# Kernel tuning notes

Measured on AMD Instinct MI355X. Metric: run time of the kernel, lower is better.

The kernel has to match this reference:

```python
import jax, jax.numpy as jnp
import numpy as np

B, S, D, H = 2, 2048, 1024, 16
HD = D // H
SCALE = HD ** -0.5

def setup_inputs() -> dict:
    key = jax.random.key(0)
    ks = jax.random.split(key, 5)
    x = jax.random.normal(ks[0], (B, S, D), dtype=jnp.float32)
    Wqkv = jax.random.normal(ks[1], (D, 3 * D), dtype=jnp.float32) * (D ** -0.5)
    bqkv = jnp.zeros((3 * D,), dtype=jnp.float32)
    Wproj = jax.random.normal(ks[2], (D, D), dtype=jnp.float32) * (D ** -0.5)
    bproj = jnp.zeros((D,), dtype=jnp.float32)
    return {"x": x, "Wqkv": Wqkv, "bqkv": bqkv, "Wproj": Wproj, "bproj": bproj}

def reference(x, Wqkv, bqkv, Wproj, bproj):
    b, s, _ = x.shape
    qkv = x @ Wqkv + bqkv                       # [B,S,3D]
    qkv = qkv.reshape(b, s, 3, H, HD)
    q, k, v = [jnp.transpose(qkv[:, :, i], (0, 2, 1, 3)) for i in range(3)]  # [B,H,S,HD]
    attn = jnp.einsum('bhqd,bhkd->bhqk', q, k) * SCALE   # [B,H,S,S]
    attn = jax.nn.softmax(attn, axis=-1)
    out = jnp.einsum('bhqk,bhkd->bhqd', attn, v)         # [B,H,S,HD]
    out = jnp.transpose(out, (0, 2, 1, 3)).reshape(b, s, D)
    return out @ Wproj + bproj
```

## Files before the change

kernel.cpp:

```cpp
#include <hip/hip_runtime.h>
#include <hip/hip_bf16.h>

#define BB 2
#define SS 2048
#define DD 1024
#define HH 16
#define HDD 64
#define MM (BB*SS)
#define NQKV (3*DD)
#define SCALE 0.125f
#define QPRESCALE 0.18033688f

typedef __bf16 bf16_t;
typedef bf16_t bf16x4 __attribute__((ext_vector_type(4)));
typedef bf16_t bf16x8 __attribute__((ext_vector_type(8)));
typedef float f32x4 __attribute__((ext_vector_type(4)));
typedef float f32x16 __attribute__((ext_vector_type(16)));

__device__ __forceinline__ void gl_lds16(const bf16_t* g, bf16_t* l) {
    __builtin_amdgcn_global_load_lds(
        (const __attribute__((address_space(1))) unsigned int*)(uintptr_t)g,
        (__attribute__((address_space(3))) unsigned int*)(uintptr_t)l,
        16, 0, 0);
}

__global__ __launch_bounds__(256) void prep(
    const float* __restrict__ x, const float* __restrict__ Wqkv,
    const float* __restrict__ Wproj, bf16_t* __restrict__ xb,
    bf16_t* __restrict__ wqkvt, bf16_t* __restrict__ wprojt)
{
    const int bx = blockIdx.x;
    if (bx < 2048) {
        int i = (bx * 256 + threadIdx.x) * 8;
        float4 a = *(const float4*)(x + i);
        float4 b = *(const float4*)(x + i + 4);
        bf16x8 v;
        v[0]=(bf16_t)a.x; v[1]=(bf16_t)a.y; v[2]=(bf16_t)a.z; v[3]=(bf16_t)a.w;
        v[4]=(bf16_t)b.x; v[5]=(bf16_t)b.y; v[6]=(bf16_t)b.z; v[7]=(bf16_t)b.w;
        *reinterpret_cast<bf16x8*>(xb + i) = v;
        return;
    }
    __shared__ float tile[32][33];
    const float* src; bf16_t* dst; int C, bxl, byl;
    if (bx < 5120) {
        int t = bx - 2048;
        byl = t / 96; bxl = t - byl * 96;
        src = Wqkv;  dst = wqkvt;  C = NQKV;
    } else {
        int t = bx - 5120;
        byl = t >> 5; bxl = t & 31;
        src = Wproj; dst = wprojt; C = DD;
    }
    const int R = DD;
    const int tx = threadIdx.x & 31, ty = threadIdx.x >> 5;
    const int r0 = byl * 32, c0 = bxl * 32;
    #pragma unroll
    for (int i = 0; i < 32; i += 8)
        tile[ty + i][tx] = src[(size_t)(r0 + ty + i) * C + c0 + tx];
    __syncthreads();
    #pragma unroll
    for (int i = 0; i < 32; i += 8)
        dst[(size_t)(c0 + ty + i) * R + r0 + tx] = (bf16_t)tile[tx][ty + i];
}

template <int MODE>
__global__ __launch_bounds__(256) void gemm_bt(
    const bf16_t* __restrict__ A, const bf16_t* __restrict__ Bt,
    const float* __restrict__ bias, float* __restrict__ outf,
    bf16_t* __restrict__ qw, bf16_t* __restrict__ kw, bf16_t* __restrict__ vtw,
    int N, int K)
{
    __shared__ __align__(16) bf16_t As[128 * 32];
    __shared__ __align__(16) bf16_t Bs[128 * 32];

    const int tid  = threadIdx.x;
    const int w    = tid >> 6;
    const int lane = tid & 63;
    const int lr   = lane & 15;
    const int quad = lane >> 4;
    const int m0   = blockIdx.y * 128;
    const int n0   = blockIdx.x * 128;
    const int wm   = w >> 1;
    const int wn   = w & 1;

    f32x4 acc[4][4];
    #pragma unroll
    for (int i = 0; i < 4; i++)
        #pragma unroll
        for (int j = 0; j < 4; j++) acc[i][j] = (f32x4){0.f, 0.f, 0.f, 0.f};

    const int stgRow = lane >> 2;
    const int stgCol = (lane & 3) * 8;
    const bf16_t* aPtr = A  + (size_t)(m0 + w * 32 + stgRow) * K + stgCol;
    const bf16_t* bPtr = Bt + (size_t)(n0 + w * 32 + stgRow) * K + stgCol;
    bf16_t* aDst = As + w * 1024;
    bf16_t* bDst = Bs + w * 1024;
    const size_t rowSkip = (size_t)16 * K;

    for (int ks = 0; ks < K; ks += 32) {
        __syncthreads();
        gl_lds16(aPtr + ks,           aDst);
        gl_lds16(aPtr + rowSkip + ks, aDst + 512);
        gl_lds16(bPtr + ks,           bDst);
        gl_lds16(bPtr + rowSkip + ks, bDst + 512);
        __syncthreads();

        bf16x8 af[4], bf[4];
        #pragma unroll
        for (int mi = 0; mi < 4; mi++)
            af[mi] = *reinterpret_cast<const bf16x8*>(&As[(wm * 64 + mi * 16 + lr) * 32 + quad * 8]);
        #pragma unroll
        for (int ni = 0; ni < 4; ni++)
            bf[ni] = *reinterpret_cast<const bf16x8*>(&Bs[(wn * 64 + ni * 16 + lr) * 32 + quad * 8]);
        #pragma unroll
        for (int mi = 0; mi < 4; mi++)
            #pragma unroll
            for (int ni = 0; ni < 4; ni++)
                acc[mi][ni] = __builtin_amdgcn_mfma_f32_16x16x32_bf16(af[mi], bf[ni], acc[mi][ni], 0, 0, 0);
    }

    #pragma unroll
    for (int mi = 0; mi < 4; mi++) {
        #pragma unroll
        for (int ni = 0; ni < 4; ni++) {
            #pragma unroll
            for (int reg = 0; reg < 4; reg++) {
                int row = m0 + wm * 64 + mi * 16 + quad * 4 + reg;
                int col = n0 + wn * 64 + ni * 16 + lr;
                float val = acc[mi][ni][reg] + bias[col];
                if constexpr (MODE == 0) {
                    int b = row >> 11, s = row & 2047;
                    int which = col >> 10, d = col & 1023;
                    int h = d >> 6, hd = d & 63;
                    size_t bh = (size_t)(b * HH + h);
                    if (which == 0)      qw[(bh * SS + s) * HDD + hd] = (bf16_t)(val * QPRESCALE);
                    else if (which == 1) kw[(bh * SS + s) * HDD + hd] = (bf16_t)val;
                    else                 vtw[(bh * HDD + hd) * SS + s] = (bf16_t)val;
                } else {
                    outf[(size_t)row * N + col] = val;
                }
            }
        }
    }
}

__global__ __launch_bounds__(256) void gemm_bt64(
    const bf16_t* __restrict__ A, const bf16_t* __restrict__ Bt,
    const float* __restrict__ bias, float* __restrict__ outf, int N, int K)
{
    __shared__ __align__(16) bf16_t As[2][64 * 32];
    __shared__ __align__(16) bf16_t Bs[2][128 * 32];

    const int tid  = threadIdx.x;
    const int w    = tid >> 6;
    const int lane = tid & 63;
    const int lr   = lane & 15;
    const int quad = lane >> 4;
    const int m0   = blockIdx.y * 64;
    const int n0   = blockIdx.x * 128;
    const int wm   = w >> 1;
    const int wn   = w & 1;

    f32x4 acc[2][4];
    #pragma unroll
    for (int i = 0; i < 2; i++)
        #pragma unroll
        for (int j = 0; j < 4; j++) acc[i][j] = (f32x4){0.f, 0.f, 0.f, 0.f};

    const int stgRow = lane >> 2;
    const int stgCol = (lane & 3) * 8;
    const bf16_t* aPtr = A  + (size_t)(m0 + w * 16 + stgRow) * K + stgCol;
    const bf16_t* bPtr = Bt + (size_t)(n0 + w * 32 + stgRow) * K + stgCol;
    const size_t rowSkip = (size_t)16 * K;

    for (int ks = 0; ks < K; ks += 64) {
        __syncthreads();
        #pragma unroll
        for (int s = 0; s < 2; s++) {
            const int ko = ks + s * 32;
            gl_lds16(aPtr + ko,           &As[s][w * 512]);
            gl_lds16(bPtr + ko,           &Bs[s][w * 1024]);
            gl_lds16(bPtr + rowSkip + ko, &Bs[s][w * 1024 + 512]);
        }
        __syncthreads();

        #pragma unroll
        for (int s = 0; s < 2; s++) {
            bf16x8 af[2], bf[4];
            #pragma unroll
            for (int mi = 0; mi < 2; mi++)
                af[mi] = *reinterpret_cast<const bf16x8*>(&As[s][(wm * 32 + mi * 16 + lr) * 32 + quad * 8]);
            #pragma unroll
            for (int ni = 0; ni < 4; ni++)
                bf[ni] = *reinterpret_cast<const bf16x8*>(&Bs[s][(wn * 64 + ni * 16 + lr) * 32 + quad * 8]);
            #pragma unroll
            for (int mi = 0; mi < 2; mi++)
                #pragma unroll
                for (int ni = 0; ni < 4; ni++)
                    acc[mi][ni] = __builtin_amdgcn_mfma_f32_16x16x32_bf16(af[mi], bf[ni], acc[mi][ni], 0, 0, 0);
        }
    }

    #pragma unroll
    for (int mi = 0; mi < 2; mi++)
        #pragma unroll
        for (int ni = 0; ni < 4; ni++)
            #pragma unroll
            for (int reg = 0; reg < 4; reg++) {
                int row = m0 + wm * 32 + mi * 16 + quad * 4 + reg;
                int col = n0 + wn * 64 + ni * 16 + lr;
                outf[(size_t)row * N + col] = acc[mi][ni][reg] + bias[col];
            }
}

__global__ __launch_bounds__(512, 4) void attn_kernel(
    const bf16_t* __restrict__ qws, const bf16_t* __restrict__ kws,
    const bf16_t* __restrict__ vtws, bf16_t* __restrict__ ob)
{
    __shared__ __align__(16) bf16_t smem[34048];
    bf16_t* Ks = smem;
    bf16_t* Vs = smem + 16640;

    const int tid  = threadIdx.x;
    const int w    = tid >> 6;
    const int g    = w >> 2;
    const int wg   = w & 3;
    const int lane = tid & 63;
    const int ln31 = lane & 31;
    const int ln5  = lane >> 5;

    const int qb = blockIdx.x;
    const int bh = blockIdx.y;
    const int b  = bh >> 4;
    const int h  = bh & 15;

    const bf16_t* Qh  = qws  + (size_t)bh * SS * HDD;
    const bf16_t* Kh  = kws  + (size_t)bh * SS * HDD;
    const bf16_t* Vth = vtws + (size_t)bh * HDD * SS;

    const int q0w    = qb * 128 + wg * 32;
    const int kvbase = g * 1024;

    bf16x8 aq[4];
    #pragma unroll
    for (int f = 0; f < 4; f++)
        aq[f] = *(const bf16x8*)(Qh + (size_t)(q0w + ln31) * HDD + f * 16 + ln5 * 8);

    const int gtid = tid & 255;
    const int sc = gtid & 7;
    const int sr = gtid >> 3;

    {
        const int ko = g * 520;
        const int vo = g * 4352;
        bf16x8 k0 = *(const bf16x8*)(Kh  + (size_t)(kvbase + sr     ) * HDD + sc * 8);
        bf16x8 k1 = *(const bf16x8*)(Kh  + (size_t)(kvbase + sr + 32) * HDD + sc * 8);
        bf16x8 v0 = *(const bf16x8*)(Vth + (size_t)(sr     ) * SS + kvbase + sc * 8);
        bf16x8 v1 = *(const bf16x8*)(Vth + (size_t)(sr + 32) * SS + kvbase + sc * 8);
        *reinterpret_cast<bf16x8*>(&Ks[(ko + sc * 65 + sr     ) * 8]) = k0;
        *reinterpret_cast<bf16x8*>(&Ks[(ko + sc * 65 + sr + 32) * 8]) = k1;
        bf16_t* vd0 = &Vs[vo + (sr     ) * 68 + sc * 8];
        bf16_t* vd1 = &Vs[vo + (sr + 32) * 68 + sc * 8];
        *reinterpret_cast<bf16x4*>(vd0)     = __builtin_shufflevector(v0, v0, 0,1,2,3);
        *reinterpret_cast<bf16x4*>(vd0 + 4) = __builtin_shufflevector(v0, v0, 4,5,6,7);
        *reinterpret_cast<bf16x4*>(vd1)     = __builtin_shufflevector(v1, v1, 0,1,2,3);
        *reinterpret_cast<bf16x4*>(vd1 + 4) = __builtin_shufflevector(v1, v1, 4,5,6,7);
    }
    __syncthreads();

    float l = 0.f;
    f32x16 o[2];
    #pragma unroll
    for (int nh = 0; nh < 2; nh++)
        #pragma unroll
        for (int r = 0; r < 16; r++) o[nh][r] = 0.f;

    int buf = 0;
    for (int it = 0; it < 16; ++it) {
        const int ko = buf * 1040 + g * 520;
        const int vo = buf * 8704 + g * 4352;

        f32x16 sfr[2];
        #pragma unroll
        for (int ni = 0; ni < 2; ni++) {
            #pragma unroll
            for (int r = 0; r < 16; r++) sfr[ni][r] = 0.f;
            #pragma unroll
            for (int f = 0; f < 4; f++) {
                bf16x8 kb = *reinterpret_cast<const bf16x8*>(
                    &Ks[(ko + (2 * f + ln5) * 65 + ni * 32 + ln31) * 8]);
                sfr[ni] = __builtin_amdgcn_mfma_f32_32x32x16_bf16(kb, aq[f], sfr[ni], 0, 0, 0);
            }
        }

        bf16x8 nk0, nk1, nv0, nv1;
        const bool more = (it + 1 < 16);
        if (more) {
            const int kvn = kvbase + (it + 1) * 64;
            nk0 = *(const bf16x8*)(Kh  + (size_t)(kvn + sr     ) * HDD + sc * 8);
            nk1 = *(const bf16x8*)(Kh  + (size_t)(kvn + sr + 32) * HDD + sc * 8);
            nv0 = *(const bf16x8*)(Vth + (size_t)(sr     ) * SS + kvn + sc * 8);
            nv1 = *(const bf16x8*)(Vth + (size_t)(sr + 32) * SS + kvn + sc * 8);
        }

        float p[2][16];
        #pragma unroll
        for (int ni = 0; ni < 2; ni++)
            #pragma unroll
            for (int r = 0; r < 16; r++) {
                p[ni][r] = __builtin_amdgcn_exp2f(sfr[ni][r]);
                l += p[ni][r];
            }

        bf16x8 ap[4];
        #pragma unroll
        for (int c16 = 0; c16 < 4; c16++)
            #pragma unroll
            for (int j = 0; j < 8; j++)
                ap[c16][j] = (bf16_t)p[c16 >> 1][(c16 & 1) * 8 + j];

        #pragma unroll
        for (int nh = 0; nh < 2; nh++) {
            const bf16_t* vrow = &Vs[vo + (nh * 32 + ln31) * 68];
            #pragma unroll
            for (int c16 = 0; c16 < 4; c16++) {
                bf16x4 lo = *(const bf16x4*)(vrow + c16 * 16 + 4 * ln5);
                bf16x4 hi = *(const bf16x4*)(vrow + c16 * 16 + 8 + 4 * ln5);
                bf16x8 vb = __builtin_shufflevector(lo, hi, 0, 1, 2, 3, 4, 5, 6, 7);
                o[nh] = __builtin_amdgcn_mfma_f32_32x32x16_bf16(ap[c16], vb, o[nh], 0, 0, 0);
            }
        }

        if (more) {
            const int ko1 = (buf ^ 1) * 1040 + g * 520;
            const int vo1 = (buf ^ 1) * 8704 + g * 4352;
            *reinterpret_cast<bf16x8*>(&Ks[(ko1 + sc * 65 + sr     ) * 8]) = nk0;
            *reinterpret_cast<bf16x8*>(&Ks[(ko1 + sc * 65 + sr + 32) * 8]) = nk1;
            bf16_t* vd0 = &Vs[vo1 + (sr     ) * 68 + sc * 8];
            bf16_t* vd1 = &Vs[vo1 + (sr + 32) * 68 + sc * 8];
            *reinterpret_cast<bf16x4*>(vd0)     = __builtin_shufflevector(nv0, nv0, 0,1,2,3);
            *reinterpret_cast<bf16x4*>(vd0 + 4) = __builtin_shufflevector(nv0, nv0, 4,5,6,7);
            *reinterpret_cast<bf16x4*>(vd1)     = __builtin_shufflevector(nv1, nv1, 0,1,2,3);
            *reinterpret_cast<bf16x4*>(vd1 + 4) = __builtin_shufflevector(nv1, nv1, 4,5,6,7);
        }
        __syncthreads();
        buf ^= 1;
    }

    l += __shfl_xor(l, 32, 64);

    __syncthreads();
    float* Of = (float*)smem;
    float* Lf = (float*)(smem + 16384);
    if (ln5 == 0) Lf[g * 128 + wg * 32 + ln31] = l;
    if (g == 1) {
        #pragma unroll
        for (int nh = 0; nh < 2; nh++)
            #pragma unroll
            for (int r = 0; r < 16; r++) {
                const int q = (r & 3) + 8 * (r >> 2) + 4 * ln5;
                Of[(wg * 32 + q) * 64 + nh * 32 + ln31] = o[nh][r];
            }
    }
    __syncthreads();
    if (g == 0) {
        float inv[16];
        #pragma unroll
        for (int r = 0; r < 16; r++) {
            const int q = (r & 3) + 8 * (r >> 2) + 4 * ln5;
            inv[r] = 1.f / (Lf[wg * 32 + q] + Lf[128 + wg * 32 + q]);
        }
        #pragma unroll
        for (int nh = 0; nh < 2; nh++)
            #pragma unroll
            for (int r = 0; r < 16; r++) {
                const int q  = (r & 3) + 8 * (r >> 2) + 4 * ln5;
                const int hd = nh * 32 + ln31;
                float val = (o[nh][r] + Of[(wg * 32 + q) * 64 + hd]) * inv[r];
                ob[((size_t)b * SS + q0w + q) * DD + h * HDD + hd] = (bf16_t)val;
            }
    }
}

extern "C" void kernel_launch(void* const* d_in, const int* in_sizes, int n_in,
                              void* d_out, int out_size, void* d_ws, size_t ws_size,
                              hipStream_t stream) {
    const float* x     = (const float*)d_in[0];
    const float* Wqkv  = (const float*)d_in[1];
    const float* bqkv  = (const float*)d_in[2];
    const float* Wproj = (const float*)d_in[3];
    const float* bproj = (const float*)d_in[4];
    float* out = (float*)d_out;

    const size_t NEL = (size_t)MM * DD;
    bf16_t* qws    = (bf16_t*)d_ws;
    bf16_t* kws    = qws  + NEL;
    bf16_t* vtws   = kws  + NEL;
    bf16_t* xb     = vtws + NEL;
    bf16_t* ows    = xb;
    bf16_t* wqkvt  = xb + NEL;
    bf16_t* wprojt = wqkvt + (size_t)NQKV * DD;

    prep<<<6144, 256, 0, stream>>>(x, Wqkv, Wproj, xb, wqkvt, wprojt);

    gemm_bt<0><<<dim3(NQKV / 128, MM / 128), 256, 0, stream>>>(
        xb, wqkvt, bqkv, nullptr, qws, kws, vtws, NQKV, DD);

    attn_kernel<<<dim3(SS / 128, BB * HH), 512, 0, stream>>>(qws, kws, vtws, ows);

    gemm_bt64<<<dim3(DD / 128, MM / 64), 256, 0, stream>>>(
        ows, wprojt, bproj, out, DD, DD);
}
```

Measured before the change: 187.6 us.

## Rewrite QKV GEMM with 256x192 tiles, double-buffered swizzled LDS and interleaved prefetch

Replaces the simple 128x128, BK=32 QKV GEMM, which synchronised twice per step with no overlap, with a 512-thread kernel using 256x192 block tiles and BK=64. LDS is double-buffered, and the next tile's global-to-LDS loads are issued in between MFMA phases. An XOR swizzle is added to avoid LDS bank conflicts, and s_setprio is raised around the MFMA bursts. The grid shrinks to 16x16=256 blocks, which roughly matches the CU count but adds wave quantisation risk, along with larger LDS use (~112KB) and higher register pressure.

Measured after the change: 192.5 us. +2.6%, slower.

```diff
diff --git a/kernel.cpp b/kernel.cpp
--- a/kernel.cpp
+++ b/kernel.cpp
@@ -22,6 +22,10 @@
         (const __attribute__((address_space(1))) unsigned int*)(uintptr_t)g,
         (__attribute__((address_space(3))) unsigned int*)(uintptr_t)l,
         16, 0, 0);
+}
+
+__device__ __forceinline__ f32x4 MF(bf16x8 a, bf16x8 b, f32x4 c) {
+    return __builtin_amdgcn_mfma_f32_16x16x32_bf16(a, b, c, 0, 0, 0);
 }
 
 __global__ __launch_bounds__(256) void prep(
@@ -63,81 +67,171 @@
         dst[(size_t)(c0 + ty + i) * R + r0 + tx] = (bf16_t)tile[tx][ty + i];
 }
 
-template <int MODE>
-__global__ __launch_bounds__(256) void gemm_bt(
+__global__ __launch_bounds__(512, 2) void gemm_qkv(
     const bf16_t* __restrict__ A, const bf16_t* __restrict__ Bt,
-    const float* __restrict__ bias, float* __restrict__ outf,
-    bf16_t* __restrict__ qw, bf16_t* __restrict__ kw, bf16_t* __restrict__ vtw,
-    int N, int K)
+    const float* __restrict__ bias,
+    bf16_t* __restrict__ qw, bf16_t* __restrict__ kw, bf16_t* __restrict__ vtw)
 {
-    __shared__ __align__(16) bf16_t As[128 * 32];
-    __shared__ __align__(16) bf16_t Bs[128 * 32];
+    constexpr int K  = DD;
+    constexpr int BM = 256, BN = 192, BK = 64;
+    constexpr int NT = K / BK;
+
+    __shared__ __align__(16) bf16_t smem[2 * BM * BK + 2 * BN * BK];
+    bf16_t* const As0 = smem;
+    bf16_t* const As1 = smem + BM * BK;
+    bf16_t* const Bs0 = smem + 2 * BM * BK;
+    bf16_t* const Bs1 = Bs0 + BN * BK;
 
     const int tid  = threadIdx.x;
     const int w    = tid >> 6;
     const int lane = tid & 63;
     const int lr   = lane & 15;
     const int quad = lane >> 4;
-    const int m0   = blockIdx.y * 128;
-    const int n0   = blockIdx.x * 128;
-    const int wm   = w >> 1;
-    const int wn   = w & 1;
-
-    f32x4 acc[4][4];
-    #pragma unroll
-    for (int i = 0; i < 4; i++)
-        #pragma unroll
-        for (int j = 0; j < 4; j++) acc[i][j] = (f32x4){0.f, 0.f, 0.f, 0.f};
-
-    const int stgRow = lane >> 2;
-    const int stgCol = (lane & 3) * 8;
-    const bf16_t* aPtr = A  + (size_t)(m0 + w * 32 + stgRow) * K + stgCol;
-    const bf16_t* bPtr = Bt + (size_t)(n0 + w * 32 + stgRow) * K + stgCol;
-    bf16_t* aDst = As + w * 1024;
-    bf16_t* bDst = Bs + w * 1024;
-    const size_t rowSkip = (size_t)16 * K;
-
-    for (int ks = 0; ks < K; ks += 32) {
-        __syncthreads();
-        gl_lds16(aPtr + ks,           aDst);
-        gl_lds16(aPtr + rowSkip + ks, aDst + 512);
-        gl_lds16(bPtr + ks,           bDst);
-        gl_lds16(bPtr + rowSkip + ks, bDst + 512);
-        __syncthreads();
-
-        bf16x8 af[4], bf[4];
-        #pragma unroll
-        for (int mi = 0; mi < 4; mi++)
-            af[mi] = *reinterpret_cast<const bf16x8*>(&As[(wm * 64 + mi * 16 + lr) * 32 + quad * 8]);
-        #pragma unroll
-        for (int ni = 0; ni < 4; ni++)
-            bf[ni] = *reinterpret_cast<const bf16x8*>(&Bs[(wn * 64 + ni * 16 + lr) * 32 + quad * 8]);
-        #pragma unroll
-        for (int mi = 0; mi < 4; mi++)
-            #pragma unroll
-            for (int ni = 0; ni < 4; ni++)
-                acc[mi][ni] = __builtin_amdgcn_mfma_f32_16x16x32_bf16(af[mi], bf[ni], acc[mi][ni], 0, 0, 0);
-    }
-
-    #pragma unroll
-    for (int mi = 0; mi < 4; mi++) {
-        #pragma unroll
-        for (int ni = 0; ni < 4; ni++) {
-            #pragma unroll
-            for (int reg = 0; reg < 4; reg++) {
-                int row = m0 + wm * 64 + mi * 16 + quad * 4 + reg;
-                int col = n0 + wn * 64 + ni * 16 + lr;
-                float val = acc[mi][ni][reg] + bias[col];
-                if constexpr (MODE == 0) {
-                    int b = row >> 11, s = row & 2047;
-                    int which = col >> 10, d = col & 1023;
-                    int h = d >> 6, hd = d & 63;
-                    size_t bh = (size_t)(b * HH + h);
+    const int wm   = w >> 2;
+    const int wn   = w & 3;
+    const int m0   = blockIdx.y * BM;
+    const int n0   = blockIdx.x * BN;
+
+    const int sx   = lr & 7;
+    const int ecc0 = ((quad)     ^ sx) * 8;
+    const int ecc1 = ((quad + 4) ^ sx) * 8;
+    const int aOff = (wm * 128 + lr) * BK;
+    const int bOff = (wn * 48  + lr) * BK;
+
+    f32x4 acc[2][4][3];
+    #pragma unroll
+    for (int mh = 0; mh < 2; mh++)
+        #pragma unroll
+        for (int mi = 0; mi < 4; mi++)
+            #pragma unroll
+            for (int ni = 0; ni < 3; ni++)
+                acc[mh][mi][ni] = (f32x4){0.f, 0.f, 0.f, 0.f};
+
+    auto stageA = [&](int kt, bf16_t* dst) {
+        #pragma unroll
+        for (int r = 0; r < 4; ++r) {
+            const int c   = r * 512 + tid;
+            const int row = c >> 3;
+            const int cg  = (c & 7) ^ (row & 7);
+            gl_lds16(A + (size_t)(m0 + row) * K + kt * BK + cg * 8, dst + c * 8);
+        }
+    };
+    auto stageB = [&](int kt, bf16_t* dst) {
+        #pragma unroll
+        for (int r = 0; r < 3; ++r) {
+            const int c   = r * 512 + tid;
+            const int row = c >> 3;
+            const int cg  = (c & 7) ^ (row & 7);
+            gl_lds16(Bt + (size_t)(n0 + row) * K + kt * BK + cg * 8, dst + c * 8);
+        }
+    };
+
+    stageA(0, As0);
+    stageB(0, Bs0);
+    asm volatile("s_waitcnt vmcnt(0)" ::: "memory");
+    __builtin_amdgcn_s_barrier();
+
+    auto tile = [&](int t, const bf16_t* Ac, const bf16_t* Bc,
+                    bf16_t* An, bf16_t* Bn) {
+        const bool more = (t + 1) < NT;
+        bf16x8 af[4], bk0[3], bk1[3];
+
+        #pragma unroll
+        for (int mi = 0; mi < 4; mi++)
+            af[mi] = *(const bf16x8*)(Ac + aOff + mi * 16 * BK + ecc0);
+        #pragma unroll
+        for (int ni = 0; ni < 3; ni++)
+            bk0[ni] = *(const bf16x8*)(Bc + bOff + ni * 16 * BK + ecc0);
+        if (more) stageA(t + 1, An);
+        __builtin_amdgcn_s_barrier();
+        __builtin_amdgcn_sched_barrier(0);
+        __builtin_amdgcn_s_setprio(1);
+        #pragma unroll
+        for (int mi = 0; mi < 4; mi++)
+            #pragma unroll
+            for (int ni = 0; ni < 3; ni++)
+                acc[0][mi][ni] = MF(af[mi], bk0[ni], acc[0][mi][ni]);
+        __builtin_amdgcn_s_setprio(0);
+        __builtin_amdgcn_sched_barrier(0);
+        __builtin_amdgcn_s_barrier();
+
+        #pragma unroll
+        for (int mi = 0; mi < 4; mi++)
+            af[mi] = *(const bf16x8*)(Ac + aOff + mi * 16 * BK + ecc1);
+        #pragma unroll
+        for (int ni = 0; ni < 3; ni++)
+            bk1[ni] = *(const bf16x8*)(Bc + bOff + ni * 16 * BK + ecc1);
+        if (more) stageB(t + 1, Bn);
+        __builtin_amdgcn_s_barrier();
+        __builtin_amdgcn_sched_barrier(0);
+        __builtin_amdgcn_s_setprio(1);
+        #pragma unroll
+        for (int mi = 0; mi < 4; mi++)
+            #pragma unroll
+            for (int ni = 0; ni < 3; ni++)
+                acc[0][mi][ni] = MF(af[mi], bk1[ni], acc[0][mi][ni]);
+        __builtin_amdgcn_s_setprio(0);
+        __builtin_amdgcn_sched_barrier(0);
+        __builtin_amdgcn_s_barrier();
+
+        #pragma unroll
+        for (int mi = 0; mi < 4; mi++)
+            af[mi] = *(const bf16x8*)(Ac + aOff + (64 + mi * 16) * BK + ecc1);
+        __builtin_amdgcn_s_barrier();
+        __builtin_amdgcn_sched_barrier(0);
+        __builtin_amdgcn_s_setprio(1);
+        #pragma unroll
+        for (int mi = 0; mi < 4; mi++)
+            #pragma unroll
+            for (int ni = 0; ni < 3; ni++)
+                acc[1][mi][ni] = MF(af[mi], bk1[ni], acc[1][mi][ni]);
+        __builtin_amdgcn_s_setprio(0);
+        __builtin_amdgcn_sched_barrier(0);
+        __builtin_amdgcn_s_barrier();
+
+        #pragma unroll
+        for (int mi = 0; mi < 4; mi++)
+            af[mi] = *(const bf16x8*)(Ac + aOff + (64 + mi * 16) * BK + ecc0);
+        __builtin_amdgcn_s_barrier();
+        __builtin_amdgcn_sched_barrier(0);
+        __builtin_amdgcn_s_setprio(1);
+        #pragma unroll
+        for (int mi = 0; mi < 4; mi++)
+            #pragma unroll
+            for (int ni = 0; ni < 3; ni++)
+                acc[1][mi][ni] = MF(af[mi], bk0[ni], acc[1][mi][ni]);
+        __builtin_amdgcn_s_setprio(0);
+        __builtin_amdgcn_sched_barrier(0);
+        if (more) asm volatile("s_waitcnt vmcnt(0)" ::: "memory");
+        __builtin_amdgcn_s_barrier();
+    };
+
+    #pragma unroll 1
+    for (int tt = 0; tt < NT; tt += 2) {
+        tile(tt,     As0, Bs0, As1, Bs1);
+        tile(tt + 1, As1, Bs1, As0, Bs0);
+    }
+
+    #pragma unroll
+    for (int mh = 0; mh < 2; mh++) {
+        #pragma unroll
+        for (int mi = 0; mi < 4; mi++) {
+            #pragma unroll
+            for (int ni = 0; ni < 3; ni++) {
+                const int col = n0 + wn * 48 + ni * 16 + lr;
+                const float bcol = bias[col];
+                const int which = col >> 10;
+                const int d = col & 1023;
+                const int h = d >> 6, hd = d & 63;
+                #pragma unroll
+                for (int reg = 0; reg < 4; reg++) {
+                    const int row = m0 + wm * 128 + mh * 64 + mi * 16 + quad * 4 + reg;
+                    const float val = acc[mh][mi][ni][reg] + bcol;
+                    const int b = row >> 11, s = row & 2047;
+                    const size_t bh = (size_t)(b * HH + h);
                     if (which == 0)      qw[(bh * SS + s) * HDD + hd] = (bf16_t)(val * QPRESCALE);
                     else if (which == 1) kw[(bh * SS + s) * HDD + hd] = (bf16_t)val;
                     else                 vtw[(bh * HDD + hd) * SS + s] = (bf16_t)val;
-                } else {
-                    outf[(size_t)row * N + col] = val;
                 }
             }
         }
@@ -403,8 +497,8 @@
 
     prep<<<6144, 256, 0, stream>>>(x, Wqkv, Wproj, xb, wqkvt, wprojt);
 
-    gemm_bt<0><<<dim3(NQKV / 128, MM / 128), 256, 0, stream>>>(
-        xb, wqkvt, bqkv, nullptr, qws, kws, vtws, NQKV, DD);
+    gemm_qkv<<<dim3(NQKV / 192, MM / 256), 512, 0, stream>>>(
+        xb, wqkvt, bqkv, qws, kws, vtws);
 
     attn_kernel<<<dim3(SS / 128, BB * HH), 512, 0, stream>>>(qws, kws, vtws, ows);
 
```
